# Kernel tuning notes

Hardware: AMD Instinct MI355X
Metric: run time of the kernel (lower is better)

## Reference

```python
import jax, jax.numpy as jnp
import numpy as np

EMBED_DIM = 1024
HEAD_DIM = 64


def setup_inputs() -> dict:
    key = jax.random.key(0)
    ks = jax.random.split(key, 7)
    s_in = EMBED_DIM ** -0.5  # torch Linear default init scale
    x = jax.random.normal(ks[0], (4, 4096, EMBED_DIM), dtype=jnp.float32)
    Wk = jax.random.uniform(ks[1], (HEAD_DIM, EMBED_DIM), jnp.float32, -s_in, s_in)
    bk = jax.random.uniform(ks[2], (HEAD_DIM,), jnp.float32, -s_in, s_in)
    Wq = jax.random.uniform(ks[3], (HEAD_DIM, EMBED_DIM), jnp.float32, -s_in, s_in)
    bq = jax.random.uniform(ks[4], (HEAD_DIM,), jnp.float32, -s_in, s_in)
    Wv = jax.random.uniform(ks[5], (HEAD_DIM, EMBED_DIM), jnp.float32, -s_in, s_in)
    bv = jax.random.uniform(ks[6], (HEAD_DIM,), jnp.float32, -s_in, s_in)
    return {"x": x, "Wq": Wq, "bq": bq, "Wk": Wk, "bk": bk, "Wv": Wv, "bv": bv}


def reference(x, Wq, bq, Wk, bk, Wv, bv):
    # torch Linear: y = x @ W.T + b
    q = jnp.einsum('btc,dc->btd', x, Wq) + bq  # [B,T,D]
    k = jnp.einsum('btc,dc->btd', x, Wk) + bk
    v = jnp.einsum('btc,dc->btd', x, Wv) + bv
    scale = HEAD_DIM ** -0.5
    # NOTE: original divides by scale (multiplies by sqrt(head_dim)) -- faithful
    scores = jnp.einsum('btd,bsd->bts', q, k) / scale  # [B,T,T]
    attn_weights = jax.nn.softmax(scores, axis=-1)
    return jnp.einsum('bts,bsd->btd', attn_weights, v)
```

## Files before the change

kernel.cpp:

```cpp
#include <hip/hip_runtime.h>

#define BATCH 4
#define SEQ   4096
#define CDIM  1024
#define DDIM  64
#define NROW  (BATCH * SEQ)
#define NSPL  8
#define SEG   (NROW * DDIM)

typedef _Float16 f16;
typedef _Float16 f16x8 __attribute__((ext_vector_type(8)));
typedef _Float16 f16x4 __attribute__((ext_vector_type(4)));
typedef __fp16   h16x2 __attribute__((ext_vector_type(2)));
typedef float    f32x4 __attribute__((ext_vector_type(4)));

#define MFMA32(a, b, c) __builtin_amdgcn_mfma_f32_16x16x32_f16((a), (b), (c), 0, 0, 0)
#define MFMA16(a, b, c) __builtin_amdgcn_mfma_f32_16x16x16f16((a), (b), (c), 0, 0, 0)

#define GLDS(g, l)                                                            \
  __builtin_amdgcn_global_load_lds((const __attribute__((address_space(1))) void*)(g), \
                                   (__attribute__((address_space(3))) void*)(l), 16, 0, 0)

#define QSCALE 11.5415603f

__device__ inline f16x8 cvt8(f32x4 a, f32x4 b) {
  h16x2 p0 = __builtin_amdgcn_cvt_pkrtz(a[0], a[1]);
  h16x2 p1 = __builtin_amdgcn_cvt_pkrtz(a[2], a[3]);
  h16x2 p2 = __builtin_amdgcn_cvt_pkrtz(b[0], b[1]);
  h16x2 p3 = __builtin_amdgcn_cvt_pkrtz(b[2], b[3]);
  f16x8 r;
  r[0] = p0[0]; r[1] = p0[1]; r[2] = p1[0]; r[3] = p1[1];
  r[4] = p2[0]; r[5] = p2[1]; r[6] = p3[0]; r[7] = p3[1];
  return r;
}

__device__ inline f16x4 cvt4(float a, float b, float c, float d) {
  h16x2 lo = __builtin_amdgcn_cvt_pkrtz(a, b);
  h16x2 hi = __builtin_amdgcn_cvt_pkrtz(c, d);
  f16x4 r;
  r[0] = lo[0]; r[1] = lo[1]; r[2] = hi[0]; r[3] = hi[1];
  return r;
}

__global__ __launch_bounds__(256) void prep_w_kernel(const float* __restrict__ Wq,
                                                     const float* __restrict__ Wk,
                                                     const float* __restrict__ Wv,
                                                     f16* __restrict__ wf2) {
  const int t = blockIdx.x * 256 + threadIdx.x;
  const int lane = t & 63;
  const int s = t >> 6;
  const int mt = s % 12, ck = s / 12;
  const int mat = mt >> 2, tile = mt & 3;
  const int n = lane & 15, quad = lane >> 4;
  const float* W = (mat == 0) ? Wq : (mat == 1) ? Wk : Wv;
  const float* src = W + (size_t)(tile * 16 + n) * CDIM + ck * 32 + quad * 8;
  const f32x4 a = *(const f32x4*)src;
  const f32x4 b = *(const f32x4*)(src + 4);
  *(f16x8*)(wf2 + (size_t)t * 8) = cvt8(a, b);
}

__global__ __launch_bounds__(256) void proj_kernel(const float* __restrict__ x,
                                                   const f16* __restrict__ wf2,
                                                   const float* __restrict__ bq,
                                                   const float* __restrict__ bk,
                                                   const float* __restrict__ bv,
                                                   f16* __restrict__ qs,
                                                   f16* __restrict__ ks,
                                                   f16* __restrict__ vc) {
  const int tid = threadIdx.x, lane = tid & 63, w = tid >> 6;
  const int n = lane & 15, quad = lane >> 4;
  const int rowbase = blockIdx.x * 32;
  const int mtb = 3 * w;

  const float* xp0 = x + (size_t)(rowbase + n) * CDIM + quad * 8;
  const float* xp1 = x + (size_t)(rowbase + 16 + n) * CDIM + quad * 8;
  const f16* wp = wf2 + (size_t)mtb * 512 + lane * 8;

  f32x4 acc[6];
#pragma unroll
  for (int i = 0; i < 6; ++i) acc[i] = (f32x4){0.f, 0.f, 0.f, 0.f};

#define LOADCK(ck, A0, C0, A1, C1, W0, W1, W2)                  \
  do {                                                          \
    const float* xq0 = xp0 + (ck) * 32;                         \
    const float* xq1 = xp1 + (ck) * 32;                         \
    A0 = *(const f32x4*)xq0; C0 = *(const f32x4*)(xq0 + 4);     \
    A1 = *(const f32x4*)xq1; C1 = *(const f32x4*)(xq1 + 4);     \
    const f16* wq = wp + (size_t)(ck) * 6144;                   \
    W0 = *(const f16x8*)(wq);                                   \
    W1 = *(const f16x8*)(wq + 512);                             \
    W2 = *(const f16x8*)(wq + 1024);                            \
  } while (0)

#define COMPCK(A0, C0, A1, C1, W0, W1, W2)                      \
  do {                                                          \
    const f16x8 fa0 = cvt8(A0, C0);                             \
    const f16x8 fa1 = cvt8(A1, C1);                             \
    acc[0] = MFMA32(fa0, W0, acc[0]);                           \
    acc[3] = MFMA32(fa1, W0, acc[3]);                           \
    acc[1] = MFMA32(fa0, W1, acc[1]);                           \
    acc[4] = MFMA32(fa1, W1, acc[4]);                           \
    acc[2] = MFMA32(fa0, W2, acc[2]);                           \
    acc[5] = MFMA32(fa1, W2, acc[5]);                           \
  } while (0)

  f32x4 a0, c0, a1, c1, b0, d0, b1, d1;
  f16x8 u0, u1, u2, v0, v1, v2;
  LOADCK(0, a0, c0, a1, c1, u0, u1, u2);
  for (int ck = 0; ck < 32; ck += 2) {
    LOADCK(ck + 1, b0, d0, b1, d1, v0, v1, v2);
    COMPCK(a0, c0, a1, c1, u0, u1, u2);
    if (ck + 2 < 32) LOADCK(ck + 2, a0, c0, a1, c1, u0, u1, u2);
    COMPCK(b0, d0, b1, d1, v0, v1, v2);
  }
#undef LOADCK
#undef COMPCK

#pragma unroll
  for (int t = 0; t < 2; ++t) {
    const int r0 = rowbase + t * 16 + quad * 4;
#pragma unroll
    for (int i2 = 0; i2 < 3; ++i2) {
      const int mt = mtb + i2;
      const int mat = mt >> 2, tile = mt & 3;
      const int d = tile * 16 + n;
      const f32x4 aa = acc[t * 3 + i2];
      if (mat == 0) {
        const float bi = bq[d];
#pragma unroll
        for (int r = 0; r < 4; ++r)
          qs[(size_t)(r0 + r) * DDIM + d] = (f16)((aa[r] + bi) * QSCALE);
      } else if (mat == 1) {
        const float bi = bk[d];
#pragma unroll
        for (int r = 0; r < 4; ++r) {
          const int tt = r0 + r;
          const int col = ((((d >> 3) ^ (tt & 7)) << 3) | (d & 7));
          ks[(size_t)tt * DDIM + col] = (f16)(aa[r] + bi);
        }
      } else {
        const float bi = bv[d];
        const int bb = r0 >> 12;
        const int tl = r0 & (SEQ - 1);
        const int ck2 = tl >> 6;
        const int bsw = (((tl & 63) >> 2) ^ n) << 2;
        *(f16x4*)(vc + ((size_t)(bb * 64 + ck2) * 64 + d) * 64 + bsw) =
            cvt4(aa[0] + bi, aa[1] + bi, aa[2] + bi, aa[3] + bi);
      }
    }
  }
}

template <int NSPLIT>
__global__ __launch_bounds__(256, 4) void attn_kernel(const f16* __restrict__ qs,
                                                      const f16* __restrict__ ks,
                                                      const f16* __restrict__ vc,
                                                      float* __restrict__ outp,
                                                      f16* __restrict__ pacc,
                                                      float* __restrict__ pm,
                                                      float* __restrict__ pl) {
  __shared__ __attribute__((aligned(16))) f16 lk[2][4096];
  __shared__ __attribute__((aligned(16))) f16 lv[2][4096];
  const int tid = threadIdx.x, lane = tid & 63, w = tid >> 6;
  const int n = lane & 15, quad = lane >> 4;
  const int split = blockIdx.x % NSPLIT;
  const int rowblk = blockIdx.x / NSPLIT;
  const int row0 = rowblk * 128 + w * 32;
  const int bb = row0 >> 12;
  const int kbase = split * (SEQ / NSPLIT);
  const int kc0 = kbase >> 6;
  const int NC = SEQ / NSPLIT / 64;

  const f16* ksb = ks + (size_t)bb * SEQ * DDIM;
  const f16* vcb = vc + (size_t)bb * 64 * 4096;

  auto issue = [&](int c, int buf) {
#pragma unroll
    for (int i = 0; i < 2; ++i) {
      const int id = 2 * w + i;
      GLDS(ksb + (size_t)(kbase + c * 64) * 64 + id * 512 + lane * 8, &lk[buf][id * 512]);
      GLDS(vcb + (size_t)(kc0 + c) * 4096 + id * 512 + lane * 8, &lv[buf][id * 512]);
    }
  };

  f16x8 qf[2][2];
#pragma unroll
  for (int g = 0; g < 2; ++g)
#pragma unroll
    for (int hh = 0; hh < 2; ++hh)
      qf[g][hh] = *(const f16x8*)(qs + (size_t)(row0 + g * 16 + n) * DDIM + hh * 32 + quad * 8);

  const int kswz = (quad ^ (n & 7)) << 3;
  int vswz[4];
#pragma unroll
  for (int st = 0; st < 4; ++st) vswz[st] = ((((st << 2) | quad) ^ n) << 2);

  f32x4 acc[2][4];
  float m[2] = {-1e30f, -1e30f}, ll[2] = {0.f, 0.f};
#pragma unroll
  for (int g = 0; g < 2; ++g)
#pragma unroll
    for (int t = 0; t < 4; ++t) acc[g][t] = (f32x4){0.f, 0.f, 0.f, 0.f};

  issue(0, 0);
  for (int c = 0; c < NC; ++c) {
    const int b = c & 1;
    __syncthreads();
    if (c + 1 < NC) issue(c + 1, b ^ 1);

    f32x4 s[2][4];
#pragma unroll
    for (int st = 0; st < 4; ++st) {
      const f16* lkr = &lk[b][(st * 16 + n) * 64];
      const f16x8 klo = *(const f16x8*)(lkr + kswz);
      const f16x8 khi = *(const f16x8*)(lkr + (kswz ^ 32));
#pragma unroll
      for (int g = 0; g < 2; ++g) {
        f32x4 z = (f32x4){0.f, 0.f, 0.f, 0.f};
        z = MFMA32(klo, qf[g][0], z);
        s[g][st] = MFMA32(khi, qf[g][1], z);
      }
    }

    f16x4 pq[2][4];
#pragma unroll
    for (int g = 0; g < 2; ++g) {
      f32x4 mx;
#pragma unroll
      for (int r = 0; r < 4; ++r)
        mx[r] = fmaxf(fmaxf(s[g][0][r], s[g][1][r]), fmaxf(s[g][2][r], s[g][3][r]));
      float mloc = fmaxf(fmaxf(mx[0], mx[1]), fmaxf(mx[2], mx[3]));
      mloc = fmaxf(mloc, __shfl_xor(mloc, 16));
      mloc = fmaxf(mloc, __shfl_xor(mloc, 32));
      const float mnew = fmaxf(m[g], mloc);
      const float alpha = __builtin_amdgcn_exp2f(m[g] - mnew);
      m[g] = mnew;
      float psum = 0.f;
#pragma unroll
      for (int st = 0; st < 4; ++st) {
        f32x4 p;
#pragma unroll
        for (int r = 0; r < 4; ++r) p[r] = __builtin_amdgcn_exp2f(s[g][st][r] - mnew);
        psum += (p[0] + p[1]) + (p[2] + p[3]);
        pq[g][st] = cvt4(p[0], p[1], p[2], p[3]);
      }
      ll[g] = ll[g] * alpha + psum;
#pragma unroll
      for (int t = 0; t < 4; ++t) acc[g][t] *= alpha;
    }

#pragma unroll
    for (int dt = 0; dt < 4; ++dt) {
      const f16* lvr = &lv[b][(dt * 16 + n) * 64];
#pragma unroll
      for (int st = 0; st < 4; ++st) {
        const f16x4 va = *(const f16x4*)(lvr + vswz[st]);
        acc[0][dt] = MFMA16(va, pq[0][st], acc[0][dt]);
        acc[1][dt] = MFMA16(va, pq[1][st], acc[1][dt]);
      }
    }
  }

  float lred[2];
#pragma unroll
  for (int g = 0; g < 2; ++g) {
    float l = ll[g];
    l += __shfl_xor(l, 16);
    l += __shfl_xor(l, 32);
    lred[g] = l;
  }

  if (NSPLIT == 1) {
#pragma unroll
    for (int g = 0; g < 2; ++g) {
      const float inv = 1.0f / lred[g];
      const int q = row0 + g * 16 + n;
#pragma unroll
      for (int t = 0; t < 4; ++t) {
        f32x4 o = acc[g][t];
#pragma unroll
        for (int r = 0; r < 4; ++r) o[r] *= inv;
        *(f32x4*)(outp + (size_t)q * DDIM + t * 16 + quad * 4) = o;
      }
    }
  } else {
#pragma unroll
    for (int g = 0; g < 2; ++g) {
      const int q = row0 + g * 16 + n;
#pragma unroll
      for (int t = 0; t < 4; ++t)
        *(f16x4*)(pacc + ((size_t)split * NROW + q) * DDIM + t * 16 + quad * 4) =
            cvt4(acc[g][t][0], acc[g][t][1], acc[g][t][2], acc[g][t][3]);
      if (quad == 0) {
        pm[split * NROW + q] = m[g];
        pl[split * NROW + q] = lred[g];
      }
    }
  }
}

template <int NSPLIT>
__global__ __launch_bounds__(256) void combine_kernel(const f16* __restrict__ pacc,
                                                      const float* __restrict__ pm,
                                                      const float* __restrict__ pl,
                                                      float* __restrict__ out) {
  const int idx = blockIdx.x * 256 + threadIdx.x;
  const int row = idx >> 4;
  const int c = (idx & 15) * 4;
  float mm = pm[row];
#pragma unroll
  for (int s = 1; s < NSPLIT; ++s) mm = fmaxf(mm, pm[s * NROW + row]);
  float L = 0.f;
  f32x4 o = (f32x4){0.f, 0.f, 0.f, 0.f};
#pragma unroll
  for (int s = 0; s < NSPLIT; ++s) {
    const float e = __builtin_amdgcn_exp2f(pm[s * NROW + row] - mm);
    L += pl[s * NROW + row] * e;
    const f16x4 a = *(const f16x4*)(pacc + ((size_t)s * NROW + row) * DDIM + c);
#pragma unroll
    for (int j = 0; j < 4; ++j) o[j] += (float)a[j] * e;
  }
  const float inv = 1.0f / L;
#pragma unroll
  for (int j = 0; j < 4; ++j) o[j] *= inv;
  *(f32x4*)(out + (size_t)row * DDIM + c) = o;
}

extern "C" void kernel_launch(void* const* d_in, const int* in_sizes, int n_in,
                              void* d_out, int out_size, void* d_ws, size_t ws_size,
                              hipStream_t stream) {
  const float* x  = (const float*)d_in[0];
  const float* Wq = (const float*)d_in[1];
  const float* bq = (const float*)d_in[2];
  const float* Wk = (const float*)d_in[3];
  const float* bk = (const float*)d_in[4];
  const float* Wv = (const float*)d_in[5];
  const float* bv = (const float*)d_in[6];
  float* out = (float*)d_out;

  f16* wf2 = (f16*)d_ws;
  f16* qs = wf2 + 3 * 65536;
  f16* ks = qs + (size_t)SEG;
  f16* vc = ks + (size_t)SEG;
  f16* pacc = vc + (size_t)SEG;
  float* pm = (float*)(pacc + (size_t)NSPL * SEG);
  float* pl = pm + (size_t)NSPL * NROW;
  const size_t need = (size_t)((char*)(pl + (size_t)NSPL * NROW) - (char*)d_ws);

  prep_w_kernel<<<dim3(96), dim3(256), 0, stream>>>(Wq, Wk, Wv, wf2);
  proj_kernel<<<dim3(512), dim3(256), 0, stream>>>(x, wf2, bq, bk, bv, qs, ks, vc);

  if (ws_size >= need) {
    attn_kernel<NSPL><<<dim3(128 * NSPL), dim3(256), 0, stream>>>(qs, ks, vc, nullptr, pacc, pm, pl);
    combine_kernel<NSPL><<<dim3(NROW * 16 / 256), dim3(256), 0, stream>>>(pacc, pm, pl, out);
  } else {
    attn_kernel<1><<<dim3(128), dim3(256), 0, stream>>>(qs, ks, vc, out, nullptr, nullptr, nullptr);
  }
}
```

Baseline: 171.7 us.

## Restructure projection kernel to cache x rows in registers across output tiles

The projection kernel now has each wave load and convert its full 16-row x slice (all 32 k-chunks) into registers once. It then loops over two groups of three output tiles, reading the weights in a new tile-major prepacked layout. The weight prep indexing is changed to match that layout, and launch bounds request two blocks per CU. The aim is to cut redundant x conversion and expose a burst of independent loads up front, at the cost of much higher register pressure and the loss of the previous double-buffered load/compute overlap.

```diff
diff --git a/kernel.cpp b/kernel.cpp
--- a/kernel.cpp
+++ b/kernel.cpp
@@ -49,7 +49,7 @@
   const int t = blockIdx.x * 256 + threadIdx.x;
   const int lane = t & 63;
   const int s = t >> 6;
-  const int mt = s % 12, ck = s / 12;
+  const int mt = s >> 5, ck = s & 31;
   const int mat = mt >> 2, tile = mt & 3;
   const int n = lane & 15, quad = lane >> 4;
   const float* W = (mat == 0) ? Wq : (mat == 1) ? Wk : Wv;
@@ -59,72 +59,53 @@
   *(f16x8*)(wf2 + (size_t)t * 8) = cvt8(a, b);
 }
 
-__global__ __launch_bounds__(256) void proj_kernel(const float* __restrict__ x,
-                                                   const f16* __restrict__ wf2,
-                                                   const float* __restrict__ bq,
-                                                   const float* __restrict__ bk,
-                                                   const float* __restrict__ bv,
-                                                   f16* __restrict__ qs,
-                                                   f16* __restrict__ ks,
-                                                   f16* __restrict__ vc) {
+__global__ __launch_bounds__(256, 2) void proj_kernel(const float* __restrict__ x,
+                                                      const f16* __restrict__ wf2,
+                                                      const float* __restrict__ bq,
+                                                      const float* __restrict__ bk,
+                                                      const float* __restrict__ bv,
+                                                      f16* __restrict__ qs,
+                                                      f16* __restrict__ ks,
+                                                      f16* __restrict__ vc) {
   const int tid = threadIdx.x, lane = tid & 63, w = tid >> 6;
   const int n = lane & 15, quad = lane >> 4;
-  const int rowbase = blockIdx.x * 32;
-  const int mtb = 3 * w;
-
-  const float* xp0 = x + (size_t)(rowbase + n) * CDIM + quad * 8;
-  const float* xp1 = x + (size_t)(rowbase + 16 + n) * CDIM + quad * 8;
-  const f16* wp = wf2 + (size_t)mtb * 512 + lane * 8;
-
-  f32x4 acc[6];
-#pragma unroll
-  for (int i = 0; i < 6; ++i) acc[i] = (f32x4){0.f, 0.f, 0.f, 0.f};
-
-#define LOADCK(ck, A0, C0, A1, C1, W0, W1, W2)                  \
-  do {                                                          \
-    const float* xq0 = xp0 + (ck) * 32;                         \
-    const float* xq1 = xp1 + (ck) * 32;                         \
-    A0 = *(const f32x4*)xq0; C0 = *(const f32x4*)(xq0 + 4);     \
-    A1 = *(const f32x4*)xq1; C1 = *(const f32x4*)(xq1 + 4);     \
-    const f16* wq = wp + (size_t)(ck) * 6144;                   \
-    W0 = *(const f16x8*)(wq);                                   \
-    W1 = *(const f16x8*)(wq + 512);                             \
-    W2 = *(const f16x8*)(wq + 1024);                            \
-  } while (0)
-
-#define COMPCK(A0, C0, A1, C1, W0, W1, W2)                      \
-  do {                                                          \
-    const f16x8 fa0 = cvt8(A0, C0);                             \
-    const f16x8 fa1 = cvt8(A1, C1);                             \
-    acc[0] = MFMA32(fa0, W0, acc[0]);                           \
-    acc[3] = MFMA32(fa1, W0, acc[3]);                           \
-    acc[1] = MFMA32(fa0, W1, acc[1]);                           \
-    acc[4] = MFMA32(fa1, W1, acc[4]);                           \
-    acc[2] = MFMA32(fa0, W2, acc[2]);                           \
-    acc[5] = MFMA32(fa1, W2, acc[5]);                           \
-  } while (0)
-
-  f32x4 a0, c0, a1, c1, b0, d0, b1, d1;
-  f16x8 u0, u1, u2, v0, v1, v2;
-  LOADCK(0, a0, c0, a1, c1, u0, u1, u2);
-  for (int ck = 0; ck < 32; ck += 2) {
-    LOADCK(ck + 1, b0, d0, b1, d1, v0, v1, v2);
-    COMPCK(a0, c0, a1, c1, u0, u1, u2);
-    if (ck + 2 < 32) LOADCK(ck + 2, a0, c0, a1, c1, u0, u1, u2);
-    COMPCK(b0, d0, b1, d1, v0, v1, v2);
-  }
-#undef LOADCK
-#undef COMPCK
-
-#pragma unroll
-  for (int t = 0; t < 2; ++t) {
-    const int r0 = rowbase + t * 16 + quad * 4;
+  const int row16 = blockIdx.x * 32 + (w & 1) * 16;
+  const int mtb = (w >> 1) * 6;
+
+  const float* xp = x + (size_t)(row16 + n) * CDIM + quad * 8;
+  f16x8 xf[32];
+#pragma unroll
+  for (int ck = 0; ck < 32; ++ck) {
+    const f32x4 a = *(const f32x4*)(xp + ck * 32);
+    const f32x4 c = *(const f32x4*)(xp + ck * 32 + 4);
+    xf[ck] = cvt8(a, c);
+  }
+
+  const f16* wl = wf2 + (size_t)lane * 8;
+#pragma unroll
+  for (int p = 0; p < 2; ++p) {
+    const int m0 = mtb + p * 3;
+    const f16* wb = wl + (size_t)m0 * 16384;
+    f32x4 acc[3];
+#pragma unroll
+    for (int i = 0; i < 3; ++i) acc[i] = (f32x4){0.f, 0.f, 0.f, 0.f};
+#pragma unroll
+    for (int ck = 0; ck < 32; ++ck) {
+      const f16x8 w0 = *(const f16x8*)(wb + ck * 512);
+      const f16x8 w1 = *(const f16x8*)(wb + 16384 + ck * 512);
+      const f16x8 w2 = *(const f16x8*)(wb + 32768 + ck * 512);
+      acc[0] = MFMA32(xf[ck], w0, acc[0]);
+      acc[1] = MFMA32(xf[ck], w1, acc[1]);
+      acc[2] = MFMA32(xf[ck], w2, acc[2]);
+    }
+
+    const int r0 = row16 + quad * 4;
 #pragma unroll
     for (int i2 = 0; i2 < 3; ++i2) {
-      const int mt = mtb + i2;
+      const int mt = m0 + i2;
       const int mat = mt >> 2, tile = mt & 3;
       const int d = tile * 16 + n;
-      const f32x4 aa = acc[t * 3 + i2];
+      const f32x4 aa = acc[i2];
       if (mat == 0) {
         const float bi = bq[d];
 #pragma unroll
```

After: 165.4 us. 1.04x faster.
